# Kernel tuning notes

Hardware: AMD Instinct MI355X
Metric: run time of the kernel (lower is better)

Reference implementation:

```python
import jax, jax.numpy as jnp
import numpy as np

VOCAB = 21128
D_WENLAN = 2048
SENT_LEN = 44  # hard-coded in original forward


def setup_inputs() -> dict:
    key = jax.random.key(0)
    ks = jax.random.split(key, 8)
    B, S, P = 32, 8, 32
    L = S * SENT_LEN  # 352
    concat_output = jax.random.normal(ks[0], (B, S, D_WENLAN), jnp.float32)
    input_ids = jax.random.randint(ks[1], (B, L), 0, VOCAB, jnp.int32)
    topic_ids = jax.random.randint(ks[2], (B, P), 0, VOCAB, jnp.int32)
    tpw_att_mask = jnp.ones((B, P), jnp.int32)
    tpw_type_ids = jnp.zeros((B, P), jnp.int32)
    attention_mask = jnp.ones((B, L), jnp.int32)
    type_ids = jax.random.randint(ks[3], (B, L), 0, 8, jnp.int32)
    token_table = jax.random.normal(ks[4], (VOCAB, D_WENLAN), jnp.float32) * 0.02
    W1 = jax.random.normal(ks[5], (D_WENLAN, 512), jnp.float32) * 0.02
    b1 = jnp.zeros((512,), jnp.float32)
    W2 = jax.random.normal(ks[6], (512, 768), jnp.float32) * 0.02
    b2 = jnp.zeros((768,), jnp.float32)
    return dict(concat_output=concat_output, input_ids=input_ids, topic_ids=topic_ids,
                tpw_att_mask=tpw_att_mask, tpw_type_ids=tpw_type_ids,
                attention_mask=attention_mask, type_ids=type_ids,
                token_table=token_table, W1=W1, b1=b1, W2=W2, b2=b2)


def reference(concat_output, input_ids, topic_ids, tpw_att_mask, tpw_type_ids,
              attention_mask, type_ids, token_table, W1, b1, W2, b2):
    B, S, D = concat_output.shape
    # vectorized replacement of the python double-loop dict lookups:
    topic_emb = token_table[topic_ids]                      # [B,P,2048]
    inp_emb = token_table[input_ids]                        # [B,L,2048]
    # scatter-add: each sentence block of 44 tokens gets its concat_output row added
    inp_emb = inp_emb.reshape(B, S, SENT_LEN, D) + concat_output[:, :, None, :]
    input_embs = jnp.concatenate([topic_emb, inp_emb.reshape(B, S * SENT_LEN, D)], axis=1)
    # projector MLP (Linear -> tanh -> Linear)
    h = jnp.tanh(jnp.einsum('btd,dk->btk', input_embs, W1) + b1)
    gpt_input_embs = jnp.einsum('btk,ke->bte', h, W2) + b2   # [B,P+L,768]
    # auxiliary concatenated tensors fed to gpt2 (is_train=True path)
    labels = jnp.concatenate([topic_ids, input_ids], axis=1)
    full_type_ids = jnp.concatenate([tpw_type_ids, type_ids], axis=1)
    full_att_mask = jnp.concatenate([tpw_att_mask, attention_mask], axis=1)
    return gpt_input_embs, labels, full_type_ids, full_att_mask
```

## Files before the change

kernel.cpp:

```cpp
#include <hip/hip_runtime.h>
#include <math.h>

typedef _Float16 half8 __attribute__((ext_vector_type(8)));
typedef float f32x4 __attribute__((ext_vector_type(4)));

#define BB 32
#define SS 8
#define PP 32
#define SENT 44
#define LL 352
#define TT 384
#define DD 2048
#define H1 512
#define H2 768
#define MM (BB*TT)
#define OUT0 (MM*H2)

#define GLL16(g, l) __builtin_amdgcn_global_load_lds( \
    (const __attribute__((address_space(1))) void*)(g), \
    (__attribute__((address_space(3))) void*)(l), 16, 0, 0)

__global__ __launch_bounds__(256) void transpose_f16_kernel(
    const float* __restrict__ src, _Float16* __restrict__ dst, int R, int C)
{
    __shared__ float tile[32][33];
    int c0 = blockIdx.x * 32;
    int r0 = blockIdx.y * 32;
    int tx = threadIdx.x & 31;
    int ty = threadIdx.x >> 5;
    #pragma unroll
    for (int i = 0; i < 4; ++i)
        tile[ty + i*8][tx] = src[(size_t)(r0 + ty + i*8) * C + c0 + tx];
    __syncthreads();
    #pragma unroll
    for (int i = 0; i < 4; ++i)
        dst[(size_t)(c0 + ty + i*8) * R + r0 + tx] = (_Float16)tile[tx][ty + i*8];
}

#define LOADA_T(S, ap, k0) {                                               \
    const float* _p = (ap) + (k0) + akq;                                   \
    float4 v0 = *(const float4*)(_p);                                      \
    float4 v1 = *(const float4*)(_p + 4);                                  \
    float4 v2 = *(const float4*)(_p + 8);                                  \
    float4 v3 = *(const float4*)(_p + 12);                                 \
    S[0]=v0.x; S[1]=v0.y; S[2]=v0.z; S[3]=v0.w;                            \
    S[4]=v1.x; S[5]=v1.y; S[6]=v1.z; S[7]=v1.w;                            \
    S[8]=v2.x; S[9]=v2.y; S[10]=v2.z; S[11]=v2.w;                          \
    S[12]=v3.x; S[13]=v3.y; S[14]=v3.z; S[15]=v3.w;                        \
}

#define WRITEA_T(S, dst) {                                                 \
    half8 h0, h1;                                                          \
    _Pragma("unroll")                                                      \
    for (int _j = 0; _j < 8; ++_j) { h0[_j] = (_Float16)S[_j];             \
                                     h1[_j] = (_Float16)S[8 + _j]; }       \
    *(half8*)&dst[(arow * 64 + akq) ^ aswz]     = h0;                      \
    *(half8*)&dst[(arow * 64 + akq + 8) ^ aswz] = h1;                      \
}

__global__ __launch_bounds__(256) void c1_kernel(
    const float*    __restrict__ concat_output,
    const _Float16* __restrict__ W1T,
    float*          __restrict__ C1)
{
    const int tid  = threadIdx.x;
    const int wid  = tid >> 6;
    const int lane = tid & 63;
    const int bm = blockIdx.x >> 2;
    const int bn = blockIdx.x & 3;

    __shared__ _Float16 As[2][64 * 64];
    __shared__ _Float16 Bs[2][128 * 64];

    const int arow = tid >> 2;
    const int akq  = (tid & 3) * 16;
    const int aswz = (arow & 7) << 3;
    const float* aptr = concat_output + (size_t)(bm * 64 + arow) * DD;

    const int rl = lane >> 3;
    const int cg = lane & 7;
    const _Float16* bsrc = W1T + (size_t)(bn * 128 + wid * 32 + rl) * DD
                               + ((cg ^ rl) << 3);

    #define C1B(buf, k0) {                                                \
        _Pragma("unroll")                                                 \
        for (int q = 0; q < 4; ++q)                                       \
            GLL16(bsrc + (size_t)q * 8 * DD + (k0),                       \
                  &Bs[buf][(wid * 4 + q) * 512]);                         \
    }

    const int wrow = (wid >> 1) * 32;
    const int wcol = (wid & 1) * 64;
    const int fr   = lane & 15;
    const int fg   = lane >> 4;

    f32x4 acc[2][4] = {};
    float a0[16], a1[16];

    C1B(0, 0);
    LOADA_T(a0, aptr, 0);
    LOADA_T(a1, aptr, 64);
    WRITEA_T(a0, As[0]);
    __syncthreads();

    #define C1_MFMA(buf) {                                                \
        _Pragma("unroll")                                                 \
        for (int kk = 0; kk < 2; ++kk) {                                  \
            half8 af[2], bf[4];                                           \
            _Pragma("unroll")                                             \
            for (int i = 0; i < 2; ++i) {                                 \
                int row = wrow + i * 16 + fr;                             \
                af[i] = *(const half8*)&As[buf][                          \
                    (row * 64 + kk * 32 + fg * 8) ^ ((row & 7) << 3)];    \
            }                                                             \
            _Pragma("unroll")                                             \
            for (int j = 0; j < 4; ++j) {                                 \
                int row = wcol + j * 16 + fr;                             \
                bf[j] = *(const half8*)&Bs[buf][                          \
                    (row * 64 + kk * 32 + fg * 8) ^ ((row & 7) << 3)];    \
            }                                                             \
            _Pragma("unroll")                                             \
            for (int i = 0; i < 2; ++i)                                   \
                _Pragma("unroll")                                         \
                for (int j = 0; j < 4; ++j)                               \
                    acc[i][j] = __builtin_amdgcn_mfma_f32_16x16x32_f16(   \
                        af[i], bf[j], acc[i][j], 0, 0, 0);                \
        }                                                                 \
    }

    for (int tt = 0; tt < 16; ++tt) {
        const int t2 = tt * 2;
        C1B(1, (t2 + 1) * 64);
        if (t2 + 2 < 32) LOADA_T(a0, aptr, (t2 + 2) * 64);
        C1_MFMA(0);
        WRITEA_T(a1, As[1]);
        __syncthreads();
        if (t2 + 2 < 32) C1B(0, (t2 + 2) * 64);
        if (t2 + 3 < 32) LOADA_T(a1, aptr, (t2 + 3) * 64);
        C1_MFMA(1);
        if (t2 + 2 < 32) WRITEA_T(a0, As[0]);
        __syncthreads();
    }

    #pragma unroll
    for (int i = 0; i < 2; ++i)
        #pragma unroll
        for (int j = 0; j < 4; ++j) {
            int col = bn * 128 + wcol + j * 16 + fr;
            #pragma unroll
            for (int r = 0; r < 4; ++r) {
                int row = bm * 64 + wrow + i * 16 + fg * 4 + r;
                C1[(size_t)row * H1 + col] = acc[i][j][r];
            }
        }
    #undef C1B
    #undef C1_MFMA
}

__global__ __launch_bounds__(256) void gemm1_kernel(
    const float*    __restrict__ token_table,
    const int*      __restrict__ topic_ids,
    const int*      __restrict__ input_ids,
    const _Float16* __restrict__ W1T,
    const float*    __restrict__ b1,
    const float*    __restrict__ C1,
    _Float16*       __restrict__ Hout)
{
    const int tid  = threadIdx.x;
    const int wid  = tid >> 6;
    const int lane = tid & 63;

    const int logical = ((blockIdx.x & 7) * 96) + (blockIdx.x >> 3);
    const int bm = logical >> 2;
    const int bn = logical & 3;

    __shared__ _Float16 As[2][64 * 64];
    __shared__ _Float16 Bs[2][128 * 64];

    const int arow = tid >> 2;
    const int akq  = (tid & 3) * 16;
    const int aswz = (arow & 7) << 3;

    const int m = bm * 64 + arow;
    const int b = m / TT;
    const int t = m % TT;
    const float* aptr;
    if (t < PP) {
        aptr = token_table + (size_t)topic_ids[b * PP + t] * DD;
    } else {
        aptr = token_table + (size_t)input_ids[b * LL + (t - PP)] * DD;
    }

    const int rl = lane >> 3;
    const int cg = lane & 7;
    const _Float16* bsrc = W1T + (size_t)(bn * 128 + wid * 32 + rl) * DD
                               + ((cg ^ rl) << 3);

    #define G1B(buf, k0) {                                                \
        _Pragma("unroll")                                                 \
        for (int q = 0; q < 4; ++q)                                       \
            GLL16(bsrc + (size_t)q * 8 * DD + (k0),                       \
                  &Bs[buf][(wid * 4 + q) * 512]);                         \
    }

    const int wrow = (wid >> 1) * 32;
    const int wcol = (wid & 1) * 64;
    const int fr   = lane & 15;
    const int fg   = lane >> 4;

    f32x4 acc[2][4] = {};
    float a0[16], a1[16];

    G1B(0, 0);
    LOADA_T(a0, aptr, 0);
    LOADA_T(a1, aptr, 64);
    WRITEA_T(a0, As[0]);
    __syncthreads();

    #define G1_MFMA(buf) {                                                \
        _Pragma("unroll")                                                 \
        for (int kk = 0; kk < 2; ++kk) {                                  \
            half8 af[2], bf[4];                                           \
            _Pragma("unroll")                                             \
            for (int i = 0; i < 2; ++i) {                                 \
                int row = wrow + i * 16 + fr;                             \
                af[i] = *(const half8*)&As[buf][                          \
                    (row * 64 + kk * 32 + fg * 8) ^ ((row & 7) << 3)];    \
            }                                                             \
            _Pragma("unroll")                                             \
            for (int j = 0; j < 4; ++j) {                                 \
                int row = wcol + j * 16 + fr;                             \
                bf[j] = *(const half8*)&Bs[buf][                          \
                    (row * 64 + kk * 32 + fg * 8) ^ ((row & 7) << 3)];    \
            }                                                             \
            _Pragma("unroll")                                             \
            for (int i = 0; i < 2; ++i)                                   \
                _Pragma("unroll")                                         \
                for (int j = 0; j < 4; ++j)                               \
                    acc[i][j] = __builtin_amdgcn_mfma_f32_16x16x32_f16(   \
                        af[i], bf[j], acc[i][j], 0, 0, 0);                \
        }                                                                 \
    }

    for (int tt = 0; tt < 16; ++tt) {
        const int t2 = tt * 2;
        G1B(1, (t2 + 1) * 64);
        if (t2 + 2 < 32) LOADA_T(a0, aptr, (t2 + 2) * 64);
        G1_MFMA(0);
        WRITEA_T(a1, As[1]);
        __syncthreads();
        if (t2 + 2 < 32) G1B(0, (t2 + 2) * 64);
        if (t2 + 3 < 32) LOADA_T(a1, aptr, (t2 + 3) * 64);
        G1_MFMA(1);
        if (t2 + 2 < 32) WRITEA_T(a0, As[0]);
        __syncthreads();
    }

    #pragma unroll
    for (int i = 0; i < 2; ++i) {
        #pragma unroll
        for (int j = 0; j < 4; ++j) {
            int col = bn * 128 + wcol + j * 16 + fr;
            float bias = b1[col];
            #pragma unroll
            for (int r = 0; r < 4; ++r) {
                int row = bm * 64 + wrow + i * 16 + fg * 4 + r;
                int rb = row / TT;
                int rt = row - rb * TT;
                float v = acc[i][j][r] + bias;
                if (rt >= PP)
                    v += C1[(size_t)(rb * SS + (rt - PP) / SENT) * H1 + col];
                Hout[(size_t)row * H1 + col] = (_Float16)tanhf(v);
            }
        }
    }
    #undef G1B
    #undef G1_MFMA
}

__global__ __launch_bounds__(256) void gemm2_kernel(
    const _Float16* __restrict__ Hin,
    const _Float16* __restrict__ W2T,
    const float*    __restrict__ b2,
    float*          __restrict__ out)
{
    const int tid  = threadIdx.x;
    const int wid  = tid >> 6;
    const int lane = tid & 63;

    const int logical = ((blockIdx.x & 7) * 64) + (blockIdx.x >> 3);
    const int bm = logical >> 2;
    const int bn = logical & 3;

    __shared__ _Float16 As[2][96 * 64];
    __shared__ _Float16 Bs[2][192 * 64];

    const int rl = lane >> 3;
    const int cg = lane & 7;
    const _Float16* asrc = Hin + (size_t)(bm * 96 + wid * 24 + rl) * H1
                               + ((cg ^ rl) << 3);
    const _Float16* bsrc = W2T + (size_t)(bn * 192 + wid * 48 + rl) * H1
                               + ((cg ^ rl) << 3);

    #define G2_ISSUE(buf, k0) {                                           \
        _Pragma("unroll")                                                 \
        for (int q = 0; q < 3; ++q)                                       \
            GLL16(asrc + (size_t)q * 8 * H1 + (k0),                       \
                  &As[buf][(wid * 3 + q) * 512]);                         \
        _Pragma("unroll")                                                 \
        for (int q = 0; q < 6; ++q)                                       \
            GLL16(bsrc + (size_t)q * 8 * H1 + (k0),                       \
                  &Bs[buf][(wid * 6 + q) * 512]);                         \
    }

    const int wrow = (wid >> 1) * 48;
    const int wcol = (wid & 1) * 96;
    const int fr   = lane & 15;
    const int fg   = lane >> 4;

    f32x4 acc[3][6] = {};

    G2_ISSUE(0, 0);

    const int NT = H1 / 64;
    for (int t = 0; t < NT; ++t) {
        __syncthreads();
        if (t + 1 < NT) G2_ISSUE((t + 1) & 1, (t + 1) * 64);
        const int cb = t & 1;
        #pragma unroll
        for (int kk = 0; kk < 2; ++kk) {
            half8 af[3], bf[6];
            #pragma unroll
            for (int i = 0; i < 3; ++i) {
                int row = wrow + i * 16 + fr;
                af[i] = *(const half8*)&As[cb][
                    (row * 64 + kk * 32 + fg * 8) ^ ((row & 7) << 3)];
            }
            #pragma unroll
            for (int j = 0; j < 6; ++j) {
                int row = wcol + j * 16 + fr;
                bf[j] = *(const half8*)&Bs[cb][
                    (row * 64 + kk * 32 + fg * 8) ^ ((row & 7) << 3)];
            }
            #pragma unroll
            for (int i = 0; i < 3; ++i)
                #pragma unroll
                for (int j = 0; j < 6; ++j)
                    acc[i][j] = __builtin_amdgcn_mfma_f32_16x16x32_f16(af[i], bf[j], acc[i][j], 0, 0, 0);
        }
    }

    #pragma unroll
    for (int i = 0; i < 3; ++i) {
        #pragma unroll
        for (int j = 0; j < 6; ++j) {
            int col = bn * 192 + wcol + j * 16 + fr;
            float bias = b2[col];
            #pragma unroll
            for (int r = 0; r < 4; ++r) {
                int row = bm * 96 + wrow + i * 16 + fg * 4 + r;
                out[(size_t)row * H2 + col] = acc[i][j][r] + bias;
            }
        }
    }
    #undef G2_ISSUE
}

__global__ __launch_bounds__(256) void aux_kernel(
    const int* __restrict__ topic_ids,
    const int* __restrict__ input_ids,
    const int* __restrict__ tpw_type_ids,
    const int* __restrict__ type_ids,
    const int* __restrict__ tpw_att_mask,
    const int* __restrict__ attention_mask,
    float* __restrict__ out)
{
    int idx = blockIdx.x * 256 + threadIdx.x;
    if (idx >= MM) return;
    int b = idx / TT, t = idx % TT;
    int lab, ty, mk;
    if (t < PP) {
        lab = topic_ids[b * PP + t];
        ty  = tpw_type_ids[b * PP + t];
        mk  = tpw_att_mask[b * PP + t];
    } else {
        int u = t - PP;
        lab = input_ids[b * LL + u];
        ty  = type_ids[b * LL + u];
        mk  = attention_mask[b * LL + u];
    }
    out[OUT0 + idx]          = (float)lab;
    out[OUT0 + MM + idx]     = (float)ty;
    out[OUT0 + 2 * MM + idx] = (float)mk;
}

extern "C" void kernel_launch(void* const* d_in, const int* in_sizes, int n_in,
                              void* d_out, int out_size, void* d_ws, size_t ws_size,
                              hipStream_t stream) {
    const float* concat_output  = (const float*)d_in[0];
    const int*   input_ids      = (const int*)d_in[1];
    const int*   topic_ids      = (const int*)d_in[2];
    const int*   tpw_att_mask   = (const int*)d_in[3];
    const int*   tpw_type_ids   = (const int*)d_in[4];
    const int*   attention_mask = (const int*)d_in[5];
    const int*   type_ids       = (const int*)d_in[6];
    const float* token_table    = (const float*)d_in[7];
    const float* W1             = (const float*)d_in[8];
    const float* b1             = (const float*)d_in[9];
    const float* W2             = (const float*)d_in[10];
    const float* b2             = (const float*)d_in[11];
    float* out = (float*)d_out;

    _Float16* w1t = (_Float16*)d_ws;
    _Float16* w2t = w1t + (size_t)H1 * DD;
    _Float16* Hws = w2t + (size_t)H2 * H1;
    float*    C1w = (float*)(Hws + (size_t)MM * H1);

    transpose_f16_kernel<<<dim3(H1 / 32, DD / 32), 256, 0, stream>>>(W1, w1t, DD, H1);
    transpose_f16_kernel<<<dim3(H2 / 32, H1 / 32), 256, 0, stream>>>(W2, w2t, H1, H2);
    aux_kernel<<<(MM + 255) / 256, 256, 0, stream>>>(
        topic_ids, input_ids, tpw_type_ids, type_ids, tpw_att_mask, attention_mask, out);
    c1_kernel<<<16, 256, 0, stream>>>(concat_output, w1t, C1w);

    gemm1_kernel<<<(MM / 64) * (H1 / 128), 256, 0, stream>>>(
        token_table, topic_ids, input_ids, w1t, b1, C1w, Hws);
    gemm2_kernel<<<(MM / 96) * (H2 / 192), 256, 0, stream>>>(Hws, w2t, b2, out);
}
```

Before: 110.4 us.

## Shrink gemm1 tiles to 64x64x32 and simplify pipeline, dropping LDS swizzle

Reworks the first GEMM from 64x128 tiles with a K-step of 64 to 64x64 tiles with a K-step of 32. This doubles the grid and uses a simpler single-buffer-swap loop without the XOR LDS swizzle. The aim is more blocks and higher occupancy, since the smaller LDS and register footprint lets more waves run. In exchange, each gathered token-table row is read twice as often across N tiles, there are twice as many barriers per K, and unswizzled LDS reads may cause bank conflicts.

```diff
diff --git a/kernel.cpp b/kernel.cpp
--- a/kernel.cpp
+++ b/kernel.cpp
@@ -170,97 +170,86 @@
     const int wid  = tid >> 6;
     const int lane = tid & 63;
 
-    const int logical = ((blockIdx.x & 7) * 96) + (blockIdx.x >> 3);
-    const int bm = logical >> 2;
-    const int bn = logical & 3;
-
-    __shared__ _Float16 As[2][64 * 64];
-    __shared__ _Float16 Bs[2][128 * 64];
+    const int logical = ((blockIdx.x & 7) * 192) + (blockIdx.x >> 3);
+    const int bm = logical >> 3;
+    const int bn = logical & 7;
+
+    __shared__ _Float16 As[2][64 * 32];
+    __shared__ _Float16 Bs[2][64 * 32];
 
     const int arow = tid >> 2;
-    const int akq  = (tid & 3) * 16;
-    const int aswz = (arow & 7) << 3;
-
+    const int akq  = (tid & 3) * 8;
     const int m = bm * 64 + arow;
     const int b = m / TT;
     const int t = m % TT;
-    const float* aptr;
-    if (t < PP) {
-        aptr = token_table + (size_t)topic_ids[b * PP + t] * DD;
-    } else {
-        aptr = token_table + (size_t)input_ids[b * LL + (t - PP)] * DD;
-    }
-
-    const int rl = lane >> 3;
-    const int cg = lane & 7;
-    const _Float16* bsrc = W1T + (size_t)(bn * 128 + wid * 32 + rl) * DD
-                               + ((cg ^ rl) << 3);
-
-    #define G1B(buf, k0) {                                                \
-        _Pragma("unroll")                                                 \
-        for (int q = 0; q < 4; ++q)                                       \
-            GLL16(bsrc + (size_t)q * 8 * DD + (k0),                       \
-                  &Bs[buf][(wid * 4 + q) * 512]);                         \
+    const int id = (t < PP) ? topic_ids[b * PP + t]
+                            : input_ids[b * LL + (t - PP)];
+    const float* aptr = token_table + (size_t)id * DD + akq;
+
+    #define LOADA(S, k0) {                                                 \
+        float4 v0 = *(const float4*)(aptr + (k0));                         \
+        float4 v1 = *(const float4*)(aptr + (k0) + 4);                     \
+        S[0]=v0.x; S[1]=v0.y; S[2]=v0.z; S[3]=v0.w;                        \
+        S[4]=v1.x; S[5]=v1.y; S[6]=v1.z; S[7]=v1.w;                        \
+    }
+    #define WRITEA(S, buf) {                                               \
+        half8 h;                                                           \
+        _Pragma("unroll")                                                  \
+        for (int _j = 0; _j < 8; ++_j) h[_j] = (_Float16)S[_j];            \
+        *(half8*)&As[buf][arow * 32 + akq] = h;                            \
+    }
+
+    const int rl = lane >> 2;
+    const int cg = lane & 3;
+    const _Float16* bsrc = W1T + (size_t)(bn * 64 + wid * 16 + rl) * DD
+                               + (cg << 3);
+
+    #define G1B(buf, k0) {                                                 \
+        GLL16(bsrc + (k0), &Bs[buf][(wid * 16) * 32]);                     \
     }
 
     const int wrow = (wid >> 1) * 32;
-    const int wcol = (wid & 1) * 64;
+    const int wcol = (wid & 1) * 32;
     const int fr   = lane & 15;
     const int fg   = lane >> 4;
 
-    f32x4 acc[2][4] = {};
-    float a0[16], a1[16];
+    f32x4 acc[2][2] = {};
+    float a[8];
 
     G1B(0, 0);
-    LOADA_T(a0, aptr, 0);
-    LOADA_T(a1, aptr, 64);
-    WRITEA_T(a0, As[0]);
+    LOADA(a, 0);
+    WRITEA(a, 0);
     __syncthreads();
 
-    #define G1_MFMA(buf) {                                                \
-        _Pragma("unroll")                                                 \
-        for (int kk = 0; kk < 2; ++kk) {                                  \
-            half8 af[2], bf[4];                                           \
-            _Pragma("unroll")                                             \
-            for (int i = 0; i < 2; ++i) {                                 \
-                int row = wrow + i * 16 + fr;                             \
-                af[i] = *(const half8*)&As[buf][                          \
-                    (row * 64 + kk * 32 + fg * 8) ^ ((row & 7) << 3)];    \
-            }                                                             \
-            _Pragma("unroll")                                             \
-            for (int j = 0; j < 4; ++j) {                                 \
-                int row = wcol + j * 16 + fr;                             \
-                bf[j] = *(const half8*)&Bs[buf][                          \
-                    (row * 64 + kk * 32 + fg * 8) ^ ((row & 7) << 3)];    \
-            }                                                             \
-            _Pragma("unroll")                                             \
-            for (int i = 0; i < 2; ++i)                                   \
-                _Pragma("unroll")                                         \
-                for (int j = 0; j < 4; ++j)                               \
-                    acc[i][j] = __builtin_amdgcn_mfma_f32_16x16x32_f16(   \
-                        af[i], bf[j], acc[i][j], 0, 0, 0);                \
-        }                                                                 \
-    }
-
-    for (int tt = 0; tt < 16; ++tt) {
-        const int t2 = tt * 2;
-        G1B(1, (t2 + 1) * 64);
-        if (t2 + 2 < 32) LOADA_T(a0, aptr, (t2 + 2) * 64);
-        G1_MFMA(0);
-        WRITEA_T(a1, As[1]);
+    const int NT = DD / 32;
+    int cur = 0;
+    for (int tt = 0; tt < NT; ++tt) {
+        if (tt + 1 < NT) { G1B(cur ^ 1, (tt + 1) * 32); LOADA(a, (tt + 1) * 32); }
+        {
+            half8 af[2], bf[2];
+            #pragma unroll
+            for (int i = 0; i < 2; ++i)
+                af[i] = *(const half8*)&As[cur][(wrow + i * 16 + fr) * 32 + fg * 8];
+            #pragma unroll
+            for (int j = 0; j < 2; ++j)
+                bf[j] = *(const half8*)&Bs[cur][(wcol + j * 16 + fr) * 32 + fg * 8];
+            #pragma unroll
+            for (int i = 0; i < 2; ++i)
+                #pragma unroll
+                for (int j = 0; j < 2; ++j)
+                    acc[i][j] = __builtin_amdgcn_mfma_f32_16x16x32_f16(
+                        af[i], bf[j], acc[i][j], 0, 0, 0);
+        }
+        if (tt + 1 < NT) WRITEA(a, cur ^ 1);
         __syncthreads();
-        if (t2 + 2 < 32) G1B(0, (t2 + 2) * 64);
-        if (t2 + 3 < 32) LOADA_T(a1, aptr, (t2 + 3) * 64);
-        G1_MFMA(1);
-        if (t2 + 2 < 32) WRITEA_T(a0, As[0]);
-        __syncthreads();
+        cur ^= 1;
     }
 
     #pragma unroll
     for (int i = 0; i < 2; ++i) {
         #pragma unroll
-        for (int j = 0; j < 4; ++j) {
-            int col = bn * 128 + wcol + j * 16 + fr;
+        for (int j = 0; j < 2; ++j) {
+            int col = bn * 64 + wcol + j * 16 + fr;
             float bias = b1[col];
             #pragma unroll
             for (int r = 0; r < 4; ++r) {
@@ -274,8 +263,9 @@
             }
         }
     }
+    #undef LOADA
+    #undef WRITEA
     #undef G1B
-    #undef G1_MFMA
 }
 
 __global__ __launch_bounds__(256) void gemm2_kernel(
@@ -422,7 +412,7 @@
         topic_ids, input_ids, tpw_type_ids, type_ids, tpw_att_mask, attention_mask, out);
     c1_kernel<<<16, 256, 0, stream>>>(concat_output, w1t, C1w);
 
-    gemm1_kernel<<<(MM / 64) * (H1 / 128), 256, 0, stream>>>(
+    gemm1_kernel<<<(MM / 64) * (H1 / 64), 256, 0, stream>>>(
         token_table, topic_ids, input_ids, w1t, b1, C1w, Hws);
     gemm2_kernel<<<(MM / 96) * (H2 / 192), 256, 0, stream>>>(Hws, w2t, b2, out);
 }
```

After: 123.9 us. 1.12x slower.
